# Optimization experiments

Measured on AMD Instinct MI355X. Metric: run time of the kernel, lower is better.

## Reference

```python
import jax, jax.numpy as jnp
import numpy as np

ANNEALING_SCALE = 0.1
BS, NV, S, D, V = 2, 16, 1024, 768, 50257

def setup_inputs() -> dict:
    key = jax.random.key(0)
    k1, k2, k3, k4, k5 = jax.random.split(key, 5)
    return {
        "input_ids": jax.random.randint(k1, (BS, S), 0, V),
        "content": jax.random.normal(k2, (BS, NV, S, D), dtype=jnp.float32),
        "contextualization": jax.random.normal(k3, (BS, NV, S, S), dtype=jnp.float32) * 0.05,
        "lm_head_weight": jax.random.normal(k4, (V, D), dtype=jnp.float32) * 0.02,
        "content_weights": jax.random.uniform(k5, (V, NV), dtype=jnp.float32),
    }

def reference(input_ids, content, contextualization, lm_head_weight, content_weights):
    bs, nv, s, d = content.shape
    # --- mask_annealing ---
    # Original computes relu(content @ W.T) over full vocab then gathers at input_ids.
    # Equivalent: gather rows of W first, then contract (same math since relu is
    # elementwise and only gathered columns are summed).
    Wg = lm_head_weight[input_ids]                              # (bs, s, d)
    sims = jnp.einsum('bkid,bjd->bkij', content, Wg)            # (bs, 16, s, s)
    sims = jnp.sum(jax.nn.relu(sims), axis=3)                   # (bs, 16, s)
    scores = jax.nn.sigmoid(-ANNEALING_SCALE * sims + 6.0)
    # upweight_nearby modifier
    scores = scores * (1.0 + jnp.arange(s, dtype=content.dtype) / 100.0)[None, None, :]
    scores = jnp.transpose(scores, (0, 2, 1))                   # (bs, s, 16)
    # --- create_content_soft_mask ---
    cw = content_weights[input_ids]                             # (bs, s, 16)
    weights = cw * scores + (1.0 - scores)                      # (bs, s, 16)
    # --- weighted sense combination ---
    content_m = content * jnp.transpose(weights, (0, 2, 1))[..., None]  # (bs,16,s,d)
    hidden = jnp.einsum('bkij,bkjd->bid', contextualization, content_m) # (bs, s, d)
    logits = hidden @ lm_head_weight.T                          # (bs, s, vocab)
    return logits
```

## Files before the change

### kernel.cpp

```cpp
#include <hip/hip_runtime.h>
#include <cstdint>
#include <cstddef>

#define BSZ 2
#define NV 16
#define SEQ 1024
#define DIM 768
#define VOC 50257
#define VOCP 50304

typedef unsigned int u32;
typedef unsigned short u16;
typedef _Float16 half8 __attribute__((ext_vector_type(8)));
typedef float f32x4 __attribute__((ext_vector_type(4)));

__device__ __forceinline__ u16 f2h(float f) {
  return __builtin_bit_cast(unsigned short, (_Float16)f);
}
__device__ __forceinline__ u32 pk2h(float a, float b) {
  return (u32)f2h(a) | ((u32)f2h(b) << 16);
}

__device__ __forceinline__ void gload16(const u16* g, u16* l) {
  __builtin_amdgcn_global_load_lds(
      (const __attribute__((address_space(1))) void*)g,
      (__attribute__((address_space(3))) void*)l, 16, 0, 0);
}

__global__ void k_prep_content(const float* __restrict__ content,
                               u16* __restrict__ cbf, u16* __restrict__ cT) {
  __shared__ u16 tile[32][33];
  const int bk = blockIdx.z;
  const int d0 = blockIdx.x * 32, j0 = blockIdx.y * 32;
  const float* src = content + (size_t)bk * SEQ * DIM;
  u16* dst = cbf + (size_t)bk * SEQ * DIM;
  u16* dstT = cT + (size_t)bk * DIM * SEQ;
  const int c = threadIdx.x;
#pragma unroll
  for (int rr = 0; rr < 4; ++rr) {
    const int r = threadIdx.y * 4 + rr;
    const float v = src[(size_t)(j0 + r) * DIM + d0 + c];
    const u16 bv = f2h(v);
    dst[(size_t)(j0 + r) * DIM + d0 + c] = bv;
    tile[r][c] = bv;
  }
  __syncthreads();
#pragma unroll
  for (int rr = 0; rr < 4; ++rr) {
    const int r = threadIdx.y * 4 + rr;
    dstT[(size_t)(d0 + r) * SEQ + j0 + c] = tile[c][r];
  }
}

__global__ void k_prep_w(const float* __restrict__ W, u16* __restrict__ Wb) {
  const int v = blockIdx.x;
  const int c = threadIdx.x * 4;
  u32 lo, hi;
  if (v < VOC) {
    const float4 f = *(const float4*)(W + (size_t)v * DIM + c);
    lo = pk2h(f.x, f.y); hi = pk2h(f.z, f.w);
  } else {
    lo = 0u; hi = 0u;
  }
  *(uint2*)(Wb + (size_t)v * DIM + c) = make_uint2(lo, hi);
}

__global__ void k_gather(const int* __restrict__ ids, const u16* __restrict__ Wb,
                         u16* __restrict__ Wg) {
  const int b = blockIdx.y, j = blockIdx.x;
  const int row = ids[b * SEQ + j];
  const int c = threadIdx.x * 4;
  *(uint2*)(Wg + ((size_t)b * SEQ + j) * DIM + c) =
      *(const uint2*)(Wb + (size_t)row * DIM + c);
}

__global__ void k_zero(float* __restrict__ p, int n) {
  const int i = blockIdx.x * 256 + threadIdx.x;
  if (i < n) p[i] = 0.f;
}

template <int LDA, int LDB>
__device__ __forceinline__ void gemm_core(const u16* __restrict__ A,
                                          const u16* __restrict__ B, int ksteps,
                                          u16* As, u16* Bs, f32x4 (&acc)[4][4],
                                          int t) {
  const int lane = t & 63, w = t >> 6, wr = w >> 1, wc = w & 1;
  const int rl = lane & 15;
  const int gsw = (((lane >> 4) ^ ((rl >> 1) & 3)) * 8);
  const int srow = 16 * w + (lane >> 2);
  const int sg = (((lane & 3) ^ ((lane >> 3) & 3)) * 8);
  const size_t gaBase = (size_t)srow * LDA + sg;
  const size_t gbBase = (size_t)srow * LDB + sg;
  u16* lA = As + w * 512;
  u16* lB = Bs + w * 512;

#define STAGE_(bb, kt)                                                  \
  {                                                                     \
    const u16* ga_ = A + gaBase + (size_t)(kt) * 32;                    \
    const u16* gb_ = B + gbBase + (size_t)(kt) * 32;                    \
    gload16(ga_, lA + (bb) * 4096);                                     \
    gload16(ga_ + (size_t)64 * LDA, lA + (bb) * 4096 + 2048);           \
    gload16(gb_, lB + (bb) * 4096);                                     \
    gload16(gb_ + (size_t)64 * LDB, lB + (bb) * 4096 + 2048);           \
  }

#define FRAGS_(bb)                                                      \
  half8 af[4], bf[4];                                                   \
  _Pragma("unroll") for (int m = 0; m < 4; ++m)                         \
      af[m] = *(const half8*)(As + (bb) * 4096 +                        \
                              (wr * 64 + m * 16 + rl) * 32 + gsw);      \
  _Pragma("unroll") for (int n = 0; n < 4; ++n)                         \
      bf[n] = *(const half8*)(Bs + (bb) * 4096 +                        \
                              (wc * 64 + n * 16 + rl) * 32 + gsw);      \
  _Pragma("unroll") for (int m = 0; m < 4; ++m)                         \
      _Pragma("unroll") for (int n = 0; n < 4; ++n)                     \
          acc[m][n] = __builtin_amdgcn_mfma_f32_16x16x32_f16(           \
              af[m], bf[n], acc[m][n], 0, 0, 0);

  STAGE_(0, 0);
  __syncthreads();
  int cur = 0;
  for (int kt = 0; kt < ksteps - 1; ++kt) {
    STAGE_(cur ^ 1, kt + 1);
    { FRAGS_(cur); }
    __syncthreads();
    cur ^= 1;
  }
  { FRAGS_(cur); }
#undef STAGE_
#undef FRAGS_
}

template <int LDA, int LDB>
__device__ __forceinline__ void gemm_ring2(const u16* __restrict__ A0,
                                           const u16* __restrict__ A1,
                                           const u16* __restrict__ B, int ksteps,
                                           u16* As0, u16* As1, u16* Bs,
                                           f32x4 (&acc0)[4][4],
                                           f32x4 (&acc1)[4][4], int t) {
  const int lane = t & 63, w = t >> 6, wr = w >> 1, wc = w & 1;
  const int rl = lane & 15;
  const int gsw = (((lane >> 4) ^ ((rl >> 1) & 3)) * 8);
  const int srow = 16 * w + (lane >> 2);
  const int sg = (((lane & 3) ^ ((lane >> 3) & 3)) * 8);
  const size_t gaBase = (size_t)srow * LDA + sg;
  const size_t gbBase = (size_t)srow * LDB + sg;
  const int wof = w * 512;

#define STG3_(ss, kt)                                                   \
  {                                                                     \
    const u16* ga0_ = A0 + gaBase + (size_t)(kt) * 32;                  \
    const u16* ga1_ = A1 + gaBase + (size_t)(kt) * 32;                  \
    const u16* gb_ = B + gbBase + (size_t)(kt) * 32;                    \
    gload16(ga0_, As0 + (ss) * 4096 + wof);                             \
    gload16(ga0_ + (size_t)64 * LDA, As0 + (ss) * 4096 + wof + 2048);   \
    gload16(ga1_, As1 + (ss) * 4096 + wof);                            \
    gload16(ga1_ + (size_t)64 * LDA, As1 + (ss) * 4096 + wof + 2048);   \
    gload16(gb_, Bs + (ss) * 4096 + wof);                              \
    gload16(gb_ + (size_t)64 * LDB, Bs + (ss) * 4096 + wof + 2048);     \
  }

#define FRAGS3_(ss)                                                     \
  half8 af0[4], af1[4], bf[4];                                          \
  _Pragma("unroll") for (int n = 0; n < 4; ++n)                         \
      bf[n] = *(const half8*)(Bs + (ss) * 4096 +                        \
                              (wc * 64 + n * 16 + rl) * 32 + gsw);      \
  _Pragma("unroll") for (int m = 0; m < 4; ++m)                         \
      af0[m] = *(const half8*)(As0 + (ss) * 4096 +                      \
                               (wr * 64 + m * 16 + rl) * 32 + gsw);     \
  _Pragma("unroll") for (int m = 0; m < 4; ++m)                         \
      af1[m] = *(const half8*)(As1 + (ss) * 4096 +                      \
                               (wr * 64 + m * 16 + rl) * 32 + gsw);

#define MFMA32_                                                         \
  __builtin_amdgcn_s_setprio(1);                                        \
  _Pragma("unroll") for (int m = 0; m < 4; ++m)                         \
      _Pragma("unroll") for (int n = 0; n < 4; ++n)                     \
          acc0[m][n] = __builtin_amdgcn_mfma_f32_16x16x32_f16(          \
              af0[m], bf[n], acc0[m][n], 0, 0, 0);                      \
  _Pragma("unroll") for (int m = 0; m < 4; ++m)                         \
      _Pragma("unroll") for (int n = 0; n < 4; ++n)                     \
          acc1[m][n] = __builtin_amdgcn_mfma_f32_16x16x32_f16(          \
              af1[m], bf[n], acc1[m][n], 0, 0, 0);                      \
  __builtin_amdgcn_s_setprio(0);

#define STEPF_(ss, kt)                                                  \
  asm volatile("s_waitcnt vmcnt(6)" ::: "memory");                      \
  __builtin_amdgcn_s_barrier();                                         \
  __builtin_amdgcn_sched_barrier(0);                                    \
  STG3_(((ss) + 2) % 3, (kt) + 2);                                      \
  { FRAGS3_(ss) MFMA32_ }

#define STEPL6_(ss)                                                     \
  asm volatile("s_waitcnt vmcnt(6)" ::: "memory");                      \
  __builtin_amdgcn_s_barrier();                                         \
  __builtin_amdgcn_sched_barrier(0);                                    \
  { FRAGS3_(ss) MFMA32_ }

#define STEPL0_(ss)                                                     \
  asm volatile("s_waitcnt vmcnt(0)" ::: "memory");                      \
  __builtin_amdgcn_s_barrier();                                         \
  __builtin_amdgcn_sched_barrier(0);                                    \
  { FRAGS3_(ss) MFMA32_ }

  STG3_(0, 0);
  STG3_(1, 1);
  const int nTrip = ksteps / 3;
  for (int u = 0; u < nTrip - 1; ++u) {
    const int kt = 3 * u;
    STEPF_(0, kt);
    STEPF_(1, kt + 1);
    STEPF_(2, kt + 2);
  }
  STEPF_(0, ksteps - 3);
  STEPL6_(1);
  STEPL0_(2);
#undef STG3_
#undef FRAGS3_
#undef MFMA32_
#undef STEPF_
#undef STEPL6_
#undef STEPL0_
}

__global__ __launch_bounds__(256, 2) void k_sims(const u16* __restrict__ cbf,
                                                 const u16* __restrict__ Wg,
                                                 float* __restrict__ sims) {
  __shared__ __align__(16) u16 As0[3 * 4096];
  __shared__ __align__(16) u16 As1[3 * 4096];
  __shared__ __align__(16) u16 Bs[3 * 4096];
  const int bk = blockIdx.z, b = bk >> 4;
  const int t = threadIdx.x;
  const int i0 = blockIdx.y * 256;
  const u16* A0 = cbf + (size_t)bk * SEQ * DIM + (size_t)i0 * DIM;
  const u16* A1 = A0 + (size_t)128 * DIM;
  const u16* B = Wg + (size_t)b * SEQ * DIM + (size_t)(blockIdx.x * 128) * DIM;
  f32x4 acc0[4][4] = {}, acc1[4][4] = {};
  gemm_ring2<DIM, DIM>(A0, A1, B, DIM / 32, As0, As1, Bs, acc0, acc1, t);
  const int lane = t & 63, w = t >> 6, wr = w >> 1;
  const int rg = lane >> 4, cl = lane & 15;
#pragma unroll
  for (int m = 0; m < 4; ++m) {
#pragma unroll
    for (int r = 0; r < 4; ++r) {
      float s0 = 0.f, s1 = 0.f;
#pragma unroll
      for (int n = 0; n < 4; ++n) {
        s0 += fmaxf(acc0[m][n][r], 0.f);
        s1 += fmaxf(acc1[m][n][r], 0.f);
      }
      s0 += __shfl_xor(s0, 1); s1 += __shfl_xor(s1, 1);
      s0 += __shfl_xor(s0, 2); s1 += __shfl_xor(s1, 2);
      s0 += __shfl_xor(s0, 4); s1 += __shfl_xor(s1, 4);
      s0 += __shfl_xor(s0, 8); s1 += __shfl_xor(s1, 8);
      if (cl == 0) {
        const int i = i0 + wr * 64 + m * 16 + rg * 4 + r;
        atomicAdd(&sims[(size_t)bk * SEQ + i], s0);
        atomicAdd(&sims[(size_t)bk * SEQ + i + 128], s1);
      }
    }
  }
}

__global__ void k_weights(const float* __restrict__ sims, const int* __restrict__ ids,
                          const float* __restrict__ cw, float* __restrict__ wtsT) {
  const int j = blockIdx.x * 256 + threadIdx.x;
  const int bk = blockIdx.y;
  const int b = bk >> 4, k = bk & 15;
  const float sm = sims[(size_t)bk * SEQ + j];
  float score = 1.f / (1.f + __expf(0.1f * sm - 6.f));
  score *= 1.f + (float)j * 0.01f;
  const int id = ids[b * SEQ + j];
  const float c = cw[(size_t)id * NV + k];
  wtsT[(size_t)bk * SEQ + j] = c * score + (1.f - score);
}

__global__ void k_ctx(const float* __restrict__ ctx, const float* __restrict__ wtsT,
                      u16* __restrict__ ctxw) {
  const size_t i = ((size_t)blockIdx.x * 256 + threadIdx.x) * 4;
  const float4 c = *(const float4*)(ctx + i);
  const size_t bk = i >> 20;
  const int j = (int)(i & (SEQ - 1));
  const float4 wv = *(const float4*)(wtsT + bk * SEQ + j);
  *(uint2*)(ctxw + i) =
      make_uint2(pk2h(c.x * wv.x, c.y * wv.y), pk2h(c.z * wv.z, c.w * wv.w));
}

__global__ __launch_bounds__(256) void k_hidden(const u16* __restrict__ ctxw,
                                                const u16* __restrict__ cT,
                                                float* __restrict__ part) {
  __shared__ __align__(16) u16 As[2 * 128 * 32];
  __shared__ __align__(16) u16 Bs[2 * 128 * 32];
  const int z = blockIdx.z;
  const int b = z >> 2, g = z & 3;
  const int i0 = blockIdx.y * 128, d0 = blockIdx.x * 128;
  const int t = threadIdx.x;
  f32x4 acc[4][4] = {};
  for (int kk = 0; kk < 4; ++kk) {
    const int sense = g * 4 + kk;
    const u16* A = ctxw + ((size_t)(b * NV + sense) * SEQ + i0) * SEQ;
    const u16* B = cT + ((size_t)(b * NV + sense) * DIM + d0) * SEQ;
    gemm_core<SEQ, SEQ>(A, B, SEQ / 32, As, Bs, acc, t);
    __syncthreads();
  }
  const int lane = t & 63, w = t >> 6, wr = w >> 1, wc = w & 1;
  const int rg = lane >> 4, cl = lane & 15;
  float* P = part + ((size_t)(g * BSZ + b) * SEQ + i0) * DIM + d0;
#pragma unroll
  for (int m = 0; m < 4; ++m)
#pragma unroll
    for (int n = 0; n < 4; ++n)
#pragma unroll
      for (int r = 0; r < 4; ++r)
        P[(size_t)(wr * 64 + m * 16 + rg * 4 + r) * DIM + wc * 64 + n * 16 + cl] =
            acc[m][n][r];
}

__global__ void k_reduce(const float* __restrict__ part, u16* __restrict__ hid) {
  const size_t i = ((size_t)blockIdx.x * 256 + threadIdx.x) * 4;
  const size_t NHID = (size_t)BSZ * SEQ * DIM;
  float4 s = {0.f, 0.f, 0.f, 0.f};
#pragma unroll
  for (int g = 0; g < 4; ++g) {
    const float4 p = *(const float4*)(part + (size_t)g * NHID + i);
    s.x += p.x; s.y += p.y; s.z += p.z; s.w += p.w;
  }
  *(uint2*)(hid + i) = make_uint2(pk2h(s.x, s.y), pk2h(s.z, s.w));
}

__global__ __launch_bounds__(512, 2) void k_logits(const u16* __restrict__ hid,
                                                   const u16* __restrict__ Wb,
                                                   float* __restrict__ out) {
  __shared__ __align__(16) u16 lds[8 * 8192];
  const int bid = blockIdx.x;
  const int swz = (bid & 7) * 197 + (bid >> 3);
  const int it = swz & 7, vt = swz >> 3;
  const int i0 = it * 256;
  const int v0 = (vt == 196) ? (VOCP - 256) : vt * 256;
  const int t = threadIdx.x;
  const int lane = t & 63, w = t >> 6;
  const int wm = w >> 2, wn = w & 3;
  const int rl = lane & 15, kg = lane >> 4;
  const int gsw = (kg ^ ((rl >> 1) & 3)) * 8;
  const int gi = w * 64 + lane;
  const int srow = gi >> 2;
  const int sgr = ((gi & 3) ^ ((srow >> 1) & 3)) * 8;
  const u16* Abase = hid + (size_t)i0 * DIM;
  const u16* Bbase = Wb + (size_t)v0 * DIM;
  u16* ldst = lds + w * 512 + lane * 8;

#define STG(slot, base, koff)                                         \
  {                                                                   \
    const u16* s_ = (base) + (size_t)srow * DIM + (koff) + sgr;       \
    gload16(s_, ldst + (slot) * 8192);                                \
    gload16(s_ + (size_t)128 * DIM, ldst + (slot) * 8192 + 4096);     \
  }

#define COMPUTE(sA, sB)                                               \
  {                                                                   \
    half8 bf[4], af[8];                                               \
    _Pragma("unroll") for (int n = 0; n < 4; ++n)                     \
        bf[n] = *(const half8*)(lds + (sB) * 8192 +                   \
                                (wn * 64 + n * 16 + rl) * 32 + gsw);  \
    _Pragma("unroll") for (int m = 0; m < 8; ++m)                     \
        af[m] = *(const half8*)(lds + (sA) * 8192 +                   \
                                (wm * 128 + m * 16 + rl) * 32 + gsw); \
    __builtin_amdgcn_s_setprio(1);                                    \
    _Pragma("unroll") for (int m = 0; m < 8; ++m)                     \
        _Pragma("unroll") for (int n = 0; n < 4; ++n)                 \
            acc[m][n] = __builtin_amdgcn_mfma_f32_16x16x32_f16(       \
                af[m], bf[n], acc[m][n], 0, 0, 0);                    \
    __builtin_amdgcn_s_setprio(0);                                    \
  }

#define WAITB(N)                                          \
  asm volatile("s_waitcnt vmcnt(" #N ")" ::: "memory");   \
  __builtin_amdgcn_s_barrier();                           \
  __builtin_amdgcn_sched_barrier(0);

  f32x4 acc[8][4] = {};
  STG(0, Abase, 0);
  STG(1, Bbase, 0);
  STG(2, Abase, 32);
  STG(3, Bbase, 32);
  STG(4, Abase, 64);
  STG(5, Bbase, 64);

  for (int tau = 0; tau < 10; ++tau) {
    const int tp = (tau & 1) * 4;
    const int kb = tau * 64;
    WAITB(8);
    STG((tp + 6) & 7, Abase, kb + 96);
    STG((tp + 7) & 7, Bbase, kb + 96);
    COMPUTE(tp, tp + 1);
    WAITB(8);
    STG((tp + 8) & 7, Abase, kb + 128);
    STG((tp + 9) & 7, Bbase, kb + 128);
    COMPUTE(tp + 2, tp + 3);
  }
  WAITB(8);
  STG(6, Abase, 736);
  STG(7, Bbase, 736);
  COMPUTE(0, 1);
  WAITB(8);
  COMPUTE(2, 3);
  WAITB(4);
  COMPUTE(4, 5);
  WAITB(0);
  COMPUTE(6, 7);
#undef STG
#undef COMPUTE
#undef WAITB

#pragma unroll
  for (int m = 0; m < 8; ++m)
#pragma unroll
    for (int n = 0; n < 4; ++n) {
      const int vv = v0 + wn * 64 + n * 16 + rl;
      if (vv < VOC) {
        const int ib = i0 + wm * 128 + m * 16 + kg * 4;
#pragma unroll
        for (int r = 0; r < 4; ++r)
          out[(size_t)(ib + r) * VOC + vv] = acc[m][n][r];
      }
    }
}

extern "C" void kernel_launch(void* const* d_in, const int* in_sizes, int n_in,
                              void* d_out, int out_size, void* d_ws, size_t ws_size,
                              hipStream_t stream) {
  const int* ids = (const int*)d_in[0];
  const float* content = (const float*)d_in[1];
  const float* ctx = (const float*)d_in[2];
  const float* W = (const float*)d_in[3];
  const float* cw = (const float*)d_in[4];
  float* out = (float*)d_out;
  char* ws = (char*)d_ws;

  u16* cbf  = (u16*)(ws);
  u16* cT   = (u16*)(ws + 50331648);
  u16* Wb   = (u16*)(ws + 100663296);
  u16* Wg   = (u16*)(ws + 177930240);
  u16* ctxw = (u16*)(ws + 181075968);
  float* sims = (float*)(ws + 248184832);
  float* wtsT = (float*)(ws + 248315904);
  float* part = (float*)cbf;
  u16* hid = Wg;

  k_prep_content<<<dim3(DIM / 32, SEQ / 32, BSZ * NV), dim3(32, 8), 0, stream>>>(
      content, cbf, cT);
  k_prep_w<<<VOCP, 192, 0, stream>>>(W, Wb);
  k_gather<<<dim3(SEQ, BSZ), 192, 0, stream>>>(ids, Wb, Wg);
  k_zero<<<128, 256, 0, stream>>>(sims, BSZ * NV * SEQ);
  k_sims<<<dim3(8, 4, BSZ * NV), 256, 0, stream>>>(cbf, Wg, sims);
  k_weights<<<dim3(4, BSZ * NV), 256, 0, stream>>>(sims, ids, cw, wtsT);
  k_ctx<<<32768, 256, 0, stream>>>(ctx, wtsT, ctxw);
  k_hidden<<<dim3(6, 8, 8), 256, 0, stream>>>(ctxw, cT, part);
  k_reduce<<<1536, 256, 0, stream>>>(part, hid);
  k_logits<<<8 * 197, 512, 0, stream>>>(hid, Wb, out);
}
```

Before: 587.1 us.

## Vectorize content transpose, triple-buffer hidden GEMM, split logits pipeline into half-slices

The content prep kernel now uses 64x64 tiles with float4 loads and 8-byte packed stores for both the fp16 copy and the transpose. The hidden GEMM replaces its double-buffered loop with a three-stage ring using explicit vmcnt waits, raw barriers, setprio around MFMAs, and launch_bounds for two blocks per CU. The logits GEMM splits each k-step into two half-slices, interleaving LDS fragment reads, global-to-LDS staging and MFMA groups with extra barriers and lgkmcnt waits. This aims to hide memory latency better, at the cost of more barriers and tighter register and LDS pressure.

```diff
diff --git a/kernel.cpp b/kernel.cpp
--- a/kernel.cpp
+++ b/kernel.cpp
@@ -29,26 +29,31 @@
 
 __global__ void k_prep_content(const float* __restrict__ content,
                                u16* __restrict__ cbf, u16* __restrict__ cT) {
-  __shared__ u16 tile[32][33];
+  __shared__ u16 tile[64][70];
   const int bk = blockIdx.z;
-  const int d0 = blockIdx.x * 32, j0 = blockIdx.y * 32;
+  const int d0 = blockIdx.x * 64, j0 = blockIdx.y * 64;
   const float* src = content + (size_t)bk * SEQ * DIM;
   u16* dst = cbf + (size_t)bk * SEQ * DIM;
   u16* dstT = cT + (size_t)bk * DIM * SEQ;
-  const int c = threadIdx.x;
-#pragma unroll
-  for (int rr = 0; rr < 4; ++rr) {
-    const int r = threadIdx.y * 4 + rr;
-    const float v = src[(size_t)(j0 + r) * DIM + d0 + c];
-    const u16 bv = f2h(v);
-    dst[(size_t)(j0 + r) * DIM + d0 + c] = bv;
-    tile[r][c] = bv;
+  const int c4 = (threadIdx.x & 15) * 4;
+  const int r0 = threadIdx.x >> 4;
+#pragma unroll
+  for (int it = 0; it < 4; ++it) {
+    const int r = it * 16 + r0;
+    const float4 f = *(const float4*)(src + (size_t)(j0 + r) * DIM + d0 + c4);
+    const u32 lo = pk2h(f.x, f.y), hi = pk2h(f.z, f.w);
+    *(uint2*)(dst + (size_t)(j0 + r) * DIM + d0 + c4) = make_uint2(lo, hi);
+    *(u32*)&tile[r][c4] = lo;
+    *(u32*)&tile[r][c4 + 2] = hi;
   }
   __syncthreads();
 #pragma unroll
-  for (int rr = 0; rr < 4; ++rr) {
-    const int r = threadIdx.y * 4 + rr;
-    dstT[(size_t)(d0 + r) * SEQ + j0 + c] = tile[c][r];
+  for (int it = 0; it < 4; ++it) {
+    const int dd = it * 16 + r0;
+    const int j4 = c4;
+    const u32 lo = (u32)tile[j4][dd] | ((u32)tile[j4 + 1][dd] << 16);
+    const u32 hi = (u32)tile[j4 + 2][dd] | ((u32)tile[j4 + 3][dd] << 16);
+    *(uint2*)(dstT + (size_t)(d0 + dd) * SEQ + j0 + j4) = make_uint2(lo, hi);
   }
 }
 
@@ -80,10 +85,10 @@
 }
 
 template <int LDA, int LDB>
-__device__ __forceinline__ void gemm_core(const u16* __restrict__ A,
-                                          const u16* __restrict__ B, int ksteps,
-                                          u16* As, u16* Bs, f32x4 (&acc)[4][4],
-                                          int t) {
+__device__ __forceinline__ void gemm_ring1(const u16* __restrict__ A,
+                                           const u16* __restrict__ B,
+                                           u16* As, u16* Bs,
+                                           f32x4 (&acc)[4][4], int t) {
   const int lane = t & 63, w = t >> 6, wr = w >> 1, wc = w & 1;
   const int rl = lane & 15;
   const int gsw = (((lane >> 4) ^ ((rl >> 1) & 3)) * 8);
@@ -91,44 +96,46 @@
   const int sg = (((lane & 3) ^ ((lane >> 3) & 3)) * 8);
   const size_t gaBase = (size_t)srow * LDA + sg;
   const size_t gbBase = (size_t)srow * LDB + sg;
-  u16* lA = As + w * 512;
-  u16* lB = Bs + w * 512;
-
-#define STAGE_(bb, kt)                                                  \
+  const int wof = w * 512;
+
+#define STG1_(ss, kt)                                                   \
   {                                                                     \
     const u16* ga_ = A + gaBase + (size_t)(kt) * 32;                    \
     const u16* gb_ = B + gbBase + (size_t)(kt) * 32;                    \
-    gload16(ga_, lA + (bb) * 4096);                                     \
-    gload16(ga_ + (size_t)64 * LDA, lA + (bb) * 4096 + 2048);           \
-    gload16(gb_, lB + (bb) * 4096);                                     \
-    gload16(gb_ + (size_t)64 * LDB, lB + (bb) * 4096 + 2048);           \
-  }
-
-#define FRAGS_(bb)                                                      \
-  half8 af[4], bf[4];                                                   \
-  _Pragma("unroll") for (int m = 0; m < 4; ++m)                         \
-      af[m] = *(const half8*)(As + (bb) * 4096 +                        \
-                              (wr * 64 + m * 16 + rl) * 32 + gsw);      \
-  _Pragma("unroll") for (int n = 0; n < 4; ++n)                         \
-      bf[n] = *(const half8*)(Bs + (bb) * 4096 +                        \
-                              (wc * 64 + n * 16 + rl) * 32 + gsw);      \
-  _Pragma("unroll") for (int m = 0; m < 4; ++m)                         \
-      _Pragma("unroll") for (int n = 0; n < 4; ++n)                     \
-          acc[m][n] = __builtin_amdgcn_mfma_f32_16x16x32_f16(           \
-              af[m], bf[n], acc[m][n], 0, 0, 0);
-
-  STAGE_(0, 0);
-  __syncthreads();
-  int cur = 0;
-  for (int kt = 0; kt < ksteps - 1; ++kt) {
-    STAGE_(cur ^ 1, kt + 1);
-    { FRAGS_(cur); }
-    __syncthreads();
-    cur ^= 1;
-  }
-  { FRAGS_(cur); }
-#undef STAGE_
-#undef FRAGS_
+    gload16(ga_, As + (ss) * 4096 + wof);                               \
+    gload16(ga_ + (size_t)64 * LDA, As + (ss) * 4096 + wof + 2048);     \
+    gload16(gb_, Bs + (ss) * 4096 + wof);                               \
+    gload16(gb_ + (size_t)64 * LDB, Bs + (ss) * 4096 + wof + 2048);     \
+  }
+
+  STG1_(0, 0);
+  STG1_(1, 1);
+#pragma unroll 1
+  for (int kt = 0; kt < 32; ++kt) {
+    if (kt < 31)
+      asm volatile("s_waitcnt vmcnt(4)" ::: "memory");
+    else
+      asm volatile("s_waitcnt vmcnt(0)" ::: "memory");
+    __builtin_amdgcn_s_barrier();
+    __builtin_amdgcn_sched_barrier(0);
+    const int ss = kt % 3;
+    if (kt < 30) STG1_((kt + 2) % 3, kt + 2);
+    half8 af[4], bf[4];
+#pragma unroll
+    for (int m = 0; m < 4; ++m)
+      af[m] = *(const half8*)(As + ss * 4096 + (wr * 64 + m * 16 + rl) * 32 + gsw);
+#pragma unroll
+    for (int n = 0; n < 4; ++n)
+      bf[n] = *(const half8*)(Bs + ss * 4096 + (wc * 64 + n * 16 + rl) * 32 + gsw);
+    __builtin_amdgcn_s_setprio(1);
+#pragma unroll
+    for (int m = 0; m < 4; ++m)
+#pragma unroll
+      for (int n = 0; n < 4; ++n)
+        acc[m][n] = __builtin_amdgcn_mfma_f32_16x16x32_f16(af[m], bf[n], acc[m][n], 0, 0, 0);
+    __builtin_amdgcn_s_setprio(0);
+  }
+#undef STG1_
 }
 
 template <int LDA, int LDB>
@@ -286,11 +293,11 @@
       make_uint2(pk2h(c.x * wv.x, c.y * wv.y), pk2h(c.z * wv.z, c.w * wv.w));
 }
 
-__global__ __launch_bounds__(256) void k_hidden(const u16* __restrict__ ctxw,
-                                                const u16* __restrict__ cT,
-                                                float* __restrict__ part) {
-  __shared__ __align__(16) u16 As[2 * 128 * 32];
-  __shared__ __align__(16) u16 Bs[2 * 128 * 32];
+__global__ __launch_bounds__(256, 2) void k_hidden(const u16* __restrict__ ctxw,
+                                                   const u16* __restrict__ cT,
+                                                   float* __restrict__ part) {
+  __shared__ __align__(16) u16 As[3 * 4096];
+  __shared__ __align__(16) u16 Bs[3 * 4096];
   const int z = blockIdx.z;
   const int b = z >> 2, g = z & 3;
   const int i0 = blockIdx.y * 128, d0 = blockIdx.x * 128;
@@ -300,7 +307,7 @@
     const int sense = g * 4 + kk;
     const u16* A = ctxw + ((size_t)(b * NV + sense) * SEQ + i0) * SEQ;
     const u16* B = cT + ((size_t)(b * NV + sense) * DIM + d0) * SEQ;
-    gemm_core<SEQ, SEQ>(A, B, SEQ / 32, As, Bs, acc, t);
+    gemm_ring1<SEQ, SEQ>(A, B, As, Bs, acc, t);
     __syncthreads();
   }
   const int lane = t & 63, w = t >> 6, wr = w >> 1, wc = w & 1;
@@ -342,9 +349,8 @@
   const int wm = w >> 2, wn = w & 3;
   const int rl = lane & 15, kg = lane >> 4;
   const int gsw = (kg ^ ((rl >> 1) & 3)) * 8;
-  const int gi = w * 64 + lane;
-  const int srow = gi >> 2;
-  const int sgr = ((gi & 3) ^ ((srow >> 1) & 3)) * 8;
+  const int srow = t >> 2;
+  const int sgr = ((t & 3) ^ ((srow >> 1) & 3)) * 8;
   const u16* Abase = hid + (size_t)i0 * DIM;
   const u16* Bbase = Wb + (size_t)v0 * DIM;
   u16* ldst = lds + w * 512 + lane * 8;
@@ -356,27 +362,58 @@
     gload16(s_ + (size_t)128 * DIM, ldst + (slot) * 8192 + 4096);     \
   }
 
-#define COMPUTE(sA, sB)                                               \
+#define SCHED0 __builtin_amdgcn_sched_barrier(0)
+#define VM8 asm volatile("s_waitcnt vmcnt(8)" ::: "memory")
+#define VM4 asm volatile("s_waitcnt vmcnt(4)" ::: "memory")
+#define VM0 asm volatile("s_waitcnt vmcnt(0)" ::: "memory")
+#define VMX
+#define LGKM0 asm volatile("s_waitcnt lgkmcnt(0)" ::: "memory"); SCHED0
+
+#define RD_BF(sB)                                                     \
+  _Pragma("unroll") for (int n = 0; n < 4; ++n)                       \
+      bf[n] = *(const half8*)(lds + (sB) * 8192 +                     \
+                              (wn * 64 + n * 16 + rl) * 32 + gsw);
+#define RD_AF(sA, mo)                                                 \
+  _Pragma("unroll") for (int m = 0; m < 4; ++m)                       \
+      af[m] = *(const half8*)(lds + (sA) * 8192 +                     \
+                              (wm * 128 + ((mo) + m) * 16 + rl) * 32 + gsw);
+#define MF16(mo)                                                      \
+  __builtin_amdgcn_s_setprio(1);                                      \
+  _Pragma("unroll") for (int m = 0; m < 4; ++m)                       \
+      _Pragma("unroll") for (int n = 0; n < 4; ++n)                   \
+          acc[(mo) + m][n] = __builtin_amdgcn_mfma_f32_16x16x32_f16(  \
+              af[m], bf[n], acc[(mo) + m][n], 0, 0, 0);               \
+  __builtin_amdgcn_s_setprio(0);
+
+#define SLICE(sA, sB, stA, stB, koff, VMW)                            \
   {                                                                   \
-    half8 bf[4], af[8];                                               \
-    _Pragma("unroll") for (int n = 0; n < 4; ++n)                     \
-        bf[n] = *(const half8*)(lds + (sB) * 8192 +                   \
-                                (wn * 64 + n * 16 + rl) * 32 + gsw);  \
-    _Pragma("unroll") for (int m = 0; m < 8; ++m)                     \
-        af[m] = *(const half8*)(lds + (sA) * 8192 +                   \
-                                (wm * 128 + m * 16 + rl) * 32 + gsw); \
-    __builtin_amdgcn_s_setprio(1);                                    \
-    _Pragma("unroll") for (int m = 0; m < 8; ++m)                     \
-        _Pragma("unroll") for (int n = 0; n < 4; ++n)                 \
-            acc[m][n] = __builtin_amdgcn_mfma_f32_16x16x32_f16(       \
-                af[m], bf[n], acc[m][n], 0, 0, 0);                    \
-    __builtin_amdgcn_s_setprio(0);                                    \
-  }
-
-#define WAITB(N)                                          \
-  asm volatile("s_waitcnt vmcnt(" #N ")" ::: "memory");   \
-  __builtin_amdgcn_s_barrier();                           \
-  __builtin_amdgcn_sched_barrier(0);
+    half8 af[4], bf[4];                                               \
+    RD_BF(sB); RD_AF(sA, 0);                                          \
+    STG(stA, Abase, koff);                                            \
+    SCHED0; __builtin_amdgcn_s_barrier();                             \
+    LGKM0; MF16(0);                                                   \
+    SCHED0; __builtin_amdgcn_s_barrier();                             \
+    RD_AF(sA, 4);                                                     \
+    STG(stB, Bbase, koff);                                            \
+    SCHED0; __builtin_amdgcn_s_barrier();                             \
+    LGKM0; MF16(4);                                                   \
+    VMW;                                                              \
+    SCHED0; __builtin_amdgcn_s_barrier();                             \
+  }
+
+#define SLICE_NS(sA, sB, VMW)                                         \
+  {                                                                   \
+    half8 af[4], bf[4];                                               \
+    RD_BF(sB); RD_AF(sA, 0);                                          \
+    SCHED0; __builtin_amdgcn_s_barrier();                             \
+    LGKM0; MF16(0);                                                   \
+    SCHED0; __builtin_amdgcn_s_barrier();                             \
+    RD_AF(sA, 4);                                                     \
+    SCHED0; __builtin_amdgcn_s_barrier();                             \
+    LGKM0; MF16(4);                                                   \
+    VMW;                                                              \
+    SCHED0; __builtin_amdgcn_s_barrier();                             \
+  }
 
   f32x4 acc[8][4] = {};
   STG(0, Abase, 0);
@@ -385,32 +422,34 @@
   STG(3, Bbase, 32);
   STG(4, Abase, 64);
   STG(5, Bbase, 64);
-
-  for (int tau = 0; tau < 10; ++tau) {
-    const int tp = (tau & 1) * 4;
-    const int kb = tau * 64;
-    WAITB(8);
-    STG((tp + 6) & 7, Abase, kb + 96);
-    STG((tp + 7) & 7, Bbase, kb + 96);
-    COMPUTE(tp, tp + 1);
-    WAITB(8);
-    STG((tp + 8) & 7, Abase, kb + 128);
-    STG((tp + 9) & 7, Bbase, kb + 128);
-    COMPUTE(tp + 2, tp + 3);
-  }
-  WAITB(8);
-  STG(6, Abase, 736);
-  STG(7, Bbase, 736);
-  COMPUTE(0, 1);
-  WAITB(8);
-  COMPUTE(2, 3);
-  WAITB(4);
-  COMPUTE(4, 5);
-  WAITB(0);
-  COMPUTE(6, 7);
+  VM8;
+  __builtin_amdgcn_s_barrier();
+  SCHED0;
+
+#pragma unroll 1
+  for (int g = 0; g < 5; ++g) {
+    const int kb = g * 128;
+    SLICE(0, 1, 6, 7, kb + 96, VM8);
+    SLICE(2, 3, 0, 1, kb + 128, VM8);
+    SLICE(4, 5, 2, 3, kb + 160, VM8);
+    SLICE(6, 7, 4, 5, kb + 192, VM8);
+  }
+  SLICE(0, 1, 6, 7, 736, VM8);
+  SLICE_NS(2, 3, VM4);
+  SLICE_NS(4, 5, VM0);
+  SLICE_NS(6, 7, VMX);
 #undef STG
-#undef COMPUTE
-#undef WAITB
+#undef SLICE
+#undef SLICE_NS
+#undef RD_BF
+#undef RD_AF
+#undef MF16
+#undef LGKM0
+#undef VM8
+#undef VM4
+#undef VM0
+#undef VMX
+#undef SCHED0
 
 #pragma unroll
   for (int m = 0; m < 8; ++m)
@@ -447,7 +486,7 @@
   float* part = (float*)cbf;
   u16* hid = Wg;
 
-  k_prep_content<<<dim3(DIM / 32, SEQ / 32, BSZ * NV), dim3(32, 8), 0, stream>>>(
+  k_prep_content<<<dim3(DIM / 64, SEQ / 64, BSZ * NV), 256, 0, stream>>>(
       content, cbf, cT);
   k_prep_w<<<VOCP, 192, 0, stream>>>(W, Wb);
   k_gather<<<dim3(SEQ, BSZ), 192, 0, stream>>>(ids, Wb, Wg);
```

Result: no change. 580.6 us (-1.1%).
